# Optimization experiments

Measured on AMD Instinct MI355X. Metric: run time of the kernel, lower is better.

Reference implementation:

```python
import jax, jax.numpy as jnp
import numpy as np

SCALE = 30.0
MARGIN = 0.5
COS_M = float(np.cos(MARGIN))
SIN_M = float(np.sin(MARGIN))
TH = float(np.cos(np.pi - MARGIN))
MM = float(np.sin(np.pi - MARGIN) * MARGIN)
LN_EPS = 1e-7

B, S, H = 16, 2048, 1024
N_SPANS = 64
N_CLASSES = 4096


def setup_inputs() -> dict:
    key = jax.random.key(0)
    k1, k2, k3, k4, k5 = jax.random.split(key, 5)
    encoder_layer = jax.random.normal(k1, (B, S, H), dtype=jnp.float32)
    ln_gamma = jnp.ones((H,), jnp.float32)
    ln_beta = jnp.zeros((H,), jnp.float32)
    # xavier-uniform-like init for arcface head weight [out, in]
    limit = float(np.sqrt(6.0 / (N_CLASSES + H)))
    arc_weight = jax.random.uniform(k2, (N_CLASSES, H), jnp.float32, -limit, limit)
    heads = jax.random.randint(k3, (B, N_SPANS), 0, S - 32).astype(jnp.int32)
    lens = jax.random.randint(k4, (B, N_SPANS), 1, 33).astype(jnp.int32)
    tails = heads + lens  # guaranteed head < tail <= S
    labels = jax.random.randint(k5, (B, N_SPANS), 0, N_CLASSES).astype(jnp.int32)
    return {
        "encoder_layer": encoder_layer,
        "ln_gamma": ln_gamma,
        "ln_beta": ln_beta,
        "arc_weight": arc_weight,
        "span_head_idxs": heads,
        "span_tail_idxs": tails,
        "labels": labels,
    }


def _span_mean(encoder_layer, heads, tails):
    # fused ragged segment-mean via inclusive prefix sums over the seq dim
    # csum: [B, S+1, H], csum[b, t] = sum of encoder_layer[b, :t]
    csum = jnp.concatenate(
        [jnp.zeros_like(encoder_layer[:, :1]), jnp.cumsum(encoder_layer, axis=1)], axis=1
    )
    gather = lambda idx: jnp.take_along_axis(csum, idx[:, :, None].astype(jnp.int32), axis=1)
    sums = gather(tails) - gather(heads)  # [B, n_spans, H]
    counts = (tails - heads).astype(encoder_layer.dtype)[:, :, None]
    return sums / counts


def _layer_norm(x, gamma, beta):
    mu = jnp.mean(x, axis=-1, keepdims=True)
    var = jnp.mean(jnp.square(x - mu), axis=-1, keepdims=True)
    return (x - mu) * jax.lax.rsqrt(var + LN_EPS) * gamma + beta


def _l2norm(x):
    return x / jnp.maximum(jnp.linalg.norm(x, axis=-1, keepdims=True), 1e-12)


def reference(encoder_layer, ln_gamma, ln_beta, arc_weight, span_head_idxs, span_tail_idxs, labels):
    emb = _span_mean(encoder_layer, span_head_idxs, span_tail_idxs)  # [B, n_spans, H]
    emb = _layer_norm(emb, ln_gamma, ln_beta)
    emb = emb.reshape(-1, emb.shape[-1])  # [B*n_spans, H]
    lab = labels.reshape(-1)
    # ArcMarginProduct: cosine similarity
    cosine = (_l2norm(emb) @ _l2norm(arc_weight).T).astype(jnp.float32)  # [N, C]
    sine = jnp.sqrt(jnp.clip(1.0 - jnp.square(cosine), 0.0))
    phi = cosine * COS_M - sine * SIN_M
    phi = jnp.where(cosine > TH, phi, cosine - MM)
    onehot = jax.nn.one_hot(lab, cosine.shape[-1], dtype=cosine.dtype)
    logits = (onehot * phi + (1.0 - onehot) * cosine) * SCALE
    # mean cross entropy (all labels valid, ignore_index unused)
    logp = jax.nn.log_softmax(logits, axis=-1)
    nll = -jnp.take_along_axis(logp, lab[:, None].astype(jnp.int32), axis=1)[:, 0]
    return jnp.mean(nll)
```

## Files before the change

kernel.cpp:

```cpp
#include <hip/hip_runtime.h>
#include <math.h>

#define B_     16
#define S_     2048
#define H_     1024
#define NS_    64
#define NC_    4096
#define NROWS  1024

#define SCALE_ 30.0f
#define COS_M_ 0.8775825618903728f
#define SIN_M_ 0.479425538604203f
#define TH_    (-0.8775825618903728f)
#define MM_    0.2397127693021015f
#define LN_EPS_ 1e-7f


__device__ __forceinline__ unsigned short f2bf(float f) {
    union { float f; unsigned int u; } v; v.f = f;
    unsigned int r = v.u + 0x7fffu + ((v.u >> 16) & 1u);
    return (unsigned short)(r >> 16);
}

__device__ __forceinline__ float block_sum(float v) {
    __shared__ float sb[4];
    #pragma unroll
    for (int off = 32; off > 0; off >>= 1) v += __shfl_down(v, off, 64);
    if ((threadIdx.x & 63) == 0) sb[threadIdx.x >> 6] = v;
    __syncthreads();
    float r = sb[0] + sb[1] + sb[2] + sb[3];
    __syncthreads();
    return r;
}

__device__ __forceinline__ float block_max(float v) {
    __shared__ float sb[4];
    #pragma unroll
    for (int off = 32; off > 0; off >>= 1) v = fmaxf(v, __shfl_down(v, off, 64));
    if ((threadIdx.x & 63) == 0) sb[threadIdx.x >> 6] = v;
    __syncthreads();
    float r = fmaxf(fmaxf(sb[0], sb[1]), fmaxf(sb[2], sb[3]));
    __syncthreads();
    return r;
}

__device__ __forceinline__ void gload16(const void* g, void* l) {
    __builtin_amdgcn_global_load_lds(
        (const __attribute__((address_space(1))) unsigned int*)g,
        (__attribute__((address_space(3))) unsigned int*)l,
        16, 0, 0);
}

typedef short bf16x8 __attribute__((ext_vector_type(8)));
typedef float f32x4  __attribute__((ext_vector_type(4)));

__global__ __launch_bounds__(256) void fused_norm_kernel(
    const float* __restrict__ enc,
    const float* __restrict__ gamma,
    const float* __restrict__ beta,
    const int*   __restrict__ heads,
    const int*   __restrict__ tails,
    const float* __restrict__ W,
    unsigned short* __restrict__ embn,
    unsigned short* __restrict__ Wn,
    unsigned int*   __restrict__ cnt)
{
    const int tid = threadIdx.x;
    if (blockIdx.x == 0 && tid == 0) *cnt = 0u;

    if (blockIdx.x < NROWS) {
        const int span = blockIdx.x;
        const int b    = span >> 6;
        const int head = heads[span];
        const int tail = tails[span];
        const int cnt_ = tail - head;

        const float4* base = (const float4*)(enc + ((size_t)b * S_ + head) * H_) + tid;
        float4 a0 = {0.f,0.f,0.f,0.f}, a1 = a0, a2 = a0, a3 = a0;
        int s = 0;
        for (; s + 4 <= cnt_; s += 4) {
            float4 x0 = base[(size_t)(s + 0) * (H_ / 4)];
            float4 x1 = base[(size_t)(s + 1) * (H_ / 4)];
            float4 x2 = base[(size_t)(s + 2) * (H_ / 4)];
            float4 x3 = base[(size_t)(s + 3) * (H_ / 4)];
            a0.x += x0.x; a0.y += x0.y; a0.z += x0.z; a0.w += x0.w;
            a1.x += x1.x; a1.y += x1.y; a1.z += x1.z; a1.w += x1.w;
            a2.x += x2.x; a2.y += x2.y; a2.z += x2.z; a2.w += x2.w;
            a3.x += x3.x; a3.y += x3.y; a3.z += x3.z; a3.w += x3.w;
        }
        for (; s < cnt_; ++s) {
            float4 x = base[(size_t)s * (H_ / 4)];
            a0.x += x.x; a0.y += x.y; a0.z += x.z; a0.w += x.w;
        }
        const float inv = 1.0f / (float)cnt_;
        float v0 = (a0.x + a1.x + a2.x + a3.x) * inv;
        float v1 = (a0.y + a1.y + a2.y + a3.y) * inv;
        float v2 = (a0.z + a1.z + a2.z + a3.z) * inv;
        float v3 = (a0.w + a1.w + a2.w + a3.w) * inv;

        float mu = block_sum(v0 + v1 + v2 + v3) * (1.0f / H_);
        float d0 = v0 - mu, d1 = v1 - mu, d2 = v2 - mu, d3 = v3 - mu;
        float var = block_sum(d0*d0 + d1*d1 + d2*d2 + d3*d3) * (1.0f / H_);
        float rstd = rsqrtf(var + LN_EPS_);

        const int h = tid * 4;
        float y0 = d0 * rstd * gamma[h+0] + beta[h+0];
        float y1 = d1 * rstd * gamma[h+1] + beta[h+1];
        float y2 = d2 * rstd * gamma[h+2] + beta[h+2];
        float y3 = d3 * rstd * gamma[h+3] + beta[h+3];

        float ss = block_sum(y0*y0 + y1*y1 + y2*y2 + y3*y3);
        float invn = 1.0f / fmaxf(sqrtf(ss), 1e-12f);

        ushort4 o;
        o.x = f2bf(y0 * invn); o.y = f2bf(y1 * invn);
        o.z = f2bf(y2 * invn); o.w = f2bf(y3 * invn);
        *(ushort4*)(embn + (size_t)span * H_ + h) = o;
    } else {
        const int row = blockIdx.x - NROWS;
        float4 x = ((const float4*)(W + (size_t)row * H_))[tid];
        float ss = block_sum(x.x*x.x + x.y*x.y + x.z*x.z + x.w*x.w);
        float invn = 1.0f / fmaxf(sqrtf(ss), 1e-12f);
        ushort4 o;
        o.x = f2bf(x.x * invn); o.y = f2bf(x.y * invn);
        o.z = f2bf(x.z * invn); o.w = f2bf(x.w * invn);
        *(ushort4*)(Wn + (size_t)row * H_ + tid * 4) = o;
    }
}

__global__ __launch_bounds__(512, 1) void gemm_kernel(
    const unsigned short* __restrict__ A,
    const unsigned short* __restrict__ Bw,
    float* __restrict__ C)
{
    __shared__ short As[3][128 * 64];
    __shared__ short Bs[3][128 * 64];

    const int bid = blockIdx.y * 8 + blockIdx.x;
    const int swz = (bid & 7) * 32 + (bid >> 3);
    const int m0  = (swz & 7) * 128;
    const int n0  = (swz >> 3) * 128;

    const int tid  = threadIdx.x;
    const int lane = tid & 63;
    const int w    = tid >> 6;
    const int wRow = (w >> 2) * 64;
    const int wCol = (w & 3) * 32;
    const int lrow = lane & 15;
    const int q    = lane >> 4;
    const int xr   = lrow & 7;

    f32x4 acc[4][2];
    #pragma unroll
    for (int i = 0; i < 4; ++i)
        #pragma unroll
        for (int j = 0; j < 2; ++j)
            acc[i][j] = (f32x4){0.f, 0.f, 0.f, 0.f};

    auto stage = [&](int bsel, int k0) {
        #pragma unroll
        for (int h = 0; h < 2; ++h) {
            const int s   = tid + h * 512;
            const int row = s >> 3;
            const int s16 = (s & 7) ^ (row & 7);
            gload16(A  + (size_t)(m0 + row) * 1024 + k0 + s16 * 8, &As[bsel][s * 8]);
            gload16(Bw + (size_t)(n0 + row) * 1024 + k0 + s16 * 8, &Bs[bsel][s * 8]);
        }
    };

    auto compute = [&](int bsel) {
        #pragma unroll
        for (int kk = 0; kk < 2; ++kk) {
            const int c16 = ((kk << 2) | q) ^ xr;
            bf16x8 af[4], bfr[2];
            #pragma unroll
            for (int i = 0; i < 4; ++i)
                af[i] = *(const bf16x8*)(&As[bsel][(wRow + i * 16 + lrow) * 64 + c16 * 8]);
            #pragma unroll
            for (int j = 0; j < 2; ++j)
                bfr[j] = *(const bf16x8*)(&Bs[bsel][(wCol + j * 16 + lrow) * 64 + c16 * 8]);
            #pragma unroll
            for (int i = 0; i < 4; ++i)
                #pragma unroll
                for (int j = 0; j < 2; ++j)
                    acc[i][j] = __builtin_amdgcn_mfma_f32_16x16x32_bf16(af[i], bfr[j], acc[i][j], 0, 0, 0);
        }
    };

    stage(0, 0);
    stage(1, 64);
    asm volatile("s_waitcnt vmcnt(4)" ::: "memory");
    __builtin_amdgcn_s_barrier();

    int cur = 0, nxt = 1, fut = 2;
    for (int t = 0; t < 14; ++t) {
        stage(fut, (t + 2) * 64);
        compute(cur);
        asm volatile("s_waitcnt vmcnt(4)" ::: "memory");
        __builtin_amdgcn_s_barrier();
        const int tmp = cur; cur = nxt; nxt = fut; fut = tmp;
    }
    compute(cur);
    asm volatile("s_waitcnt vmcnt(0)" ::: "memory");
    __builtin_amdgcn_s_barrier();
    compute(nxt);

    #pragma unroll
    for (int i = 0; i < 4; ++i) {
        const int rbase = m0 + wRow + i * 16 + q * 4;
        #pragma unroll
        for (int j = 0; j < 2; ++j) {
            const int col = n0 + wCol + j * 16 + lrow;
            #pragma unroll
            for (int r2 = 0; r2 < 4; ++r2)
                C[(size_t)(rbase + r2) * NC_ + col] = acc[i][j][r2];
        }
    }
}

__global__ __launch_bounds__(256) void ce_kernel(
    const float* __restrict__ cosine,
    const int*   __restrict__ labels,
    float* __restrict__ nll,
    float* __restrict__ out,
    unsigned int* __restrict__ cnt)
{
    __shared__ float s_lab;
    __shared__ int   s_last;
    const int row = blockIdx.x;
    const int lab = labels[row];
    const int tid = threadIdx.x;
    const float4* c4 = (const float4*)(cosine + (size_t)row * NC_);

    float vals[16];
    float m = -1e30f;
    #pragma unroll
    for (int t = 0; t < 4; ++t) {
        float4 x = c4[tid + t * 256];
        const int cbase = (tid + t * 256) * 4;
        float xs[4] = {x.x, x.y, x.z, x.w};
        #pragma unroll
        for (int k = 0; k < 4; ++k) {
            float c = xs[k];
            float logit = c;
            if (cbase + k == lab) {
                float sine = sqrtf(fmaxf(1.0f - c * c, 0.0f));
                float phi  = c * COS_M_ - sine * SIN_M_;
                logit = (c > TH_) ? phi : (c - MM_);
            }
            logit *= SCALE_;
            vals[t * 4 + k] = logit;
            if (cbase + k == lab) s_lab = logit;
            m = fmaxf(m, logit);
        }
    }
    float gm = block_max(m);
    float e = 0.f;
    #pragma unroll
    for (int t = 0; t < 16; ++t) e += expf(vals[t] - gm);
    float se = block_sum(e);

    if (tid == 0) {
        nll[row] = logf(se) + gm - s_lab;
        __threadfence();
        s_last = (atomicAdd(cnt, 1u) == NROWS - 1);
    }
    __syncthreads();
    if (s_last) {
        __threadfence();
        float s = 0.f;
        #pragma unroll
        for (int t = 0; t < 4; ++t) s += nll[tid + t * 256];
        float tot = block_sum(s);
        if (tid == 0) out[0] = tot * (1.0f / NROWS);
    }
}

extern "C" void kernel_launch(void* const* d_in, const int* in_sizes, int n_in,
                              void* d_out, int out_size, void* d_ws, size_t ws_size,
                              hipStream_t stream) {
    const float* enc    = (const float*)d_in[0];
    const float* gamma  = (const float*)d_in[1];
    const float* beta   = (const float*)d_in[2];
    const float* W      = (const float*)d_in[3];
    const int*   heads  = (const int*)d_in[4];
    const int*   tails  = (const int*)d_in[5];
    const int*   labels = (const int*)d_in[6];
    float* out = (float*)d_out;

    char* ws = (char*)d_ws;
    unsigned short* embn   = (unsigned short*)(ws);
    unsigned short* Wn     = (unsigned short*)(ws + (2u  << 20));
    float*          cosine = (float*)        (ws + (10u << 20));
    float*          nllbuf = (float*)        (ws + (26u << 20));
    unsigned int*   cnt    = (unsigned int*) (ws + (26u << 20) + 8192);

    fused_norm_kernel<<<NROWS + NC_, 256, 0, stream>>>(enc, gamma, beta, heads, tails, W, embn, Wn, cnt);
    dim3 g3(8, 32);
    gemm_kernel <<<g3,  512, 0, stream>>>(embn, Wn, cosine);
    ce_kernel   <<<NROWS, 256, 0, stream>>>(cosine, labels, nllbuf, out, cnt);
}
```

Measured before the change: 234.8 us.

## Restructure GEMM to 4 waves with 64x64 warp tiles and double buffering

The GEMM now runs 256-thread blocks in which each wave computes a 64x64 tile, up from 64x32, so each fragment loaded from LDS feeds more MFMAs. Shared-memory staging drops from triple to double buffering and waits on all outstanding loads before each barrier, which allows two blocks per CU. The LayerNorm gamma and beta reads are also vectorised into float4 loads. Fewer waves per block and a full vmcnt(0) wait may expose more load latency. The 256-tile grid is small relative to the CU count.

```diff
diff --git a/kernel.cpp b/kernel.cpp
--- a/kernel.cpp
+++ b/kernel.cpp
@@ -103,11 +103,12 @@
         float var = block_sum(d0*d0 + d1*d1 + d2*d2 + d3*d3) * (1.0f / H_);
         float rstd = rsqrtf(var + LN_EPS_);
 
-        const int h = tid * 4;
-        float y0 = d0 * rstd * gamma[h+0] + beta[h+0];
-        float y1 = d1 * rstd * gamma[h+1] + beta[h+1];
-        float y2 = d2 * rstd * gamma[h+2] + beta[h+2];
-        float y3 = d3 * rstd * gamma[h+3] + beta[h+3];
+        const float4 g4 = ((const float4*)gamma)[tid];
+        const float4 b4 = ((const float4*)beta)[tid];
+        float y0 = d0 * rstd * g4.x + b4.x;
+        float y1 = d1 * rstd * g4.y + b4.y;
+        float y2 = d2 * rstd * g4.z + b4.z;
+        float y3 = d3 * rstd * g4.w + b4.w;
 
         float ss = block_sum(y0*y0 + y1*y1 + y2*y2 + y3*y3);
         float invn = 1.0f / fmaxf(sqrtf(ss), 1e-12f);
@@ -115,7 +116,7 @@
         ushort4 o;
         o.x = f2bf(y0 * invn); o.y = f2bf(y1 * invn);
         o.z = f2bf(y2 * invn); o.w = f2bf(y3 * invn);
-        *(ushort4*)(embn + (size_t)span * H_ + h) = o;
+        *(ushort4*)(embn + (size_t)span * H_ + tid * 4) = o;
     } else {
         const int row = blockIdx.x - NROWS;
         float4 x = ((const float4*)(W + (size_t)row * H_))[tid];
@@ -128,13 +129,13 @@
     }
 }
 
-__global__ __launch_bounds__(512, 1) void gemm_kernel(
+__global__ __launch_bounds__(256, 2) void gemm_kernel(
     const unsigned short* __restrict__ A,
     const unsigned short* __restrict__ Bw,
     float* __restrict__ C)
 {
-    __shared__ short As[3][128 * 64];
-    __shared__ short Bs[3][128 * 64];
+    __shared__ short As[2][128 * 64];
+    __shared__ short Bs[2][128 * 64];
 
     const int bid = blockIdx.y * 8 + blockIdx.x;
     const int swz = (bid & 7) * 32 + (bid >> 3);
@@ -144,23 +145,23 @@
     const int tid  = threadIdx.x;
     const int lane = tid & 63;
     const int w    = tid >> 6;
-    const int wRow = (w >> 2) * 64;
-    const int wCol = (w & 3) * 32;
+    const int wm   = (w & 1) * 64;
+    const int wn   = (w >> 1) * 64;
     const int lrow = lane & 15;
     const int q    = lane >> 4;
     const int xr   = lrow & 7;
 
-    f32x4 acc[4][2];
+    f32x4 acc[4][4];
     #pragma unroll
     for (int i = 0; i < 4; ++i)
         #pragma unroll
-        for (int j = 0; j < 2; ++j)
+        for (int j = 0; j < 4; ++j)
             acc[i][j] = (f32x4){0.f, 0.f, 0.f, 0.f};
 
     auto stage = [&](int bsel, int k0) {
         #pragma unroll
-        for (int h = 0; h < 2; ++h) {
-            const int s   = tid + h * 512;
+        for (int h = 0; h < 4; ++h) {
+            const int s   = tid + h * 256;
             const int row = s >> 3;
             const int s16 = (s & 7) ^ (row & 7);
             gload16(A  + (size_t)(m0 + row) * 1024 + k0 + s16 * 8, &As[bsel][s * 8]);
@@ -172,45 +173,41 @@
         #pragma unroll
         for (int kk = 0; kk < 2; ++kk) {
             const int c16 = ((kk << 2) | q) ^ xr;
-            bf16x8 af[4], bfr[2];
+            bf16x8 af[4], bfr[4];
             #pragma unroll
             for (int i = 0; i < 4; ++i)
-                af[i] = *(const bf16x8*)(&As[bsel][(wRow + i * 16 + lrow) * 64 + c16 * 8]);
-            #pragma unroll
-            for (int j = 0; j < 2; ++j)
-                bfr[j] = *(const bf16x8*)(&Bs[bsel][(wCol + j * 16 + lrow) * 64 + c16 * 8]);
+                af[i] = *(const bf16x8*)(&As[bsel][(wm + i * 16 + lrow) * 64 + c16 * 8]);
+            #pragma unroll
+            for (int j = 0; j < 4; ++j)
+                bfr[j] = *(const bf16x8*)(&Bs[bsel][(wn + j * 16 + lrow) * 64 + c16 * 8]);
             #pragma unroll
             for (int i = 0; i < 4; ++i)
                 #pragma unroll
-                for (int j = 0; j < 2; ++j)
+                for (int j = 0; j < 4; ++j)
                     acc[i][j] = __builtin_amdgcn_mfma_f32_16x16x32_bf16(af[i], bfr[j], acc[i][j], 0, 0, 0);
         }
     };
 
     stage(0, 0);
-    stage(1, 64);
-    asm volatile("s_waitcnt vmcnt(4)" ::: "memory");
-    __builtin_amdgcn_s_barrier();
-
-    int cur = 0, nxt = 1, fut = 2;
-    for (int t = 0; t < 14; ++t) {
-        stage(fut, (t + 2) * 64);
-        compute(cur);
-        asm volatile("s_waitcnt vmcnt(4)" ::: "memory");
-        __builtin_amdgcn_s_barrier();
-        const int tmp = cur; cur = nxt; nxt = fut; fut = tmp;
-    }
-    compute(cur);
     asm volatile("s_waitcnt vmcnt(0)" ::: "memory");
     __builtin_amdgcn_s_barrier();
-    compute(nxt);
+
+    int cur = 0;
+    for (int t = 0; t < 15; ++t) {
+        stage(cur ^ 1, (t + 1) * 64);
+        compute(cur);
+        asm volatile("s_waitcnt vmcnt(0)" ::: "memory");
+        __builtin_amdgcn_s_barrier();
+        cur ^= 1;
+    }
+    compute(cur);
 
     #pragma unroll
     for (int i = 0; i < 4; ++i) {
-        const int rbase = m0 + wRow + i * 16 + q * 4;
-        #pragma unroll
-        for (int j = 0; j < 2; ++j) {
-            const int col = n0 + wCol + j * 16 + lrow;
+        const int rbase = m0 + wm + i * 16 + q * 4;
+        #pragma unroll
+        for (int j = 0; j < 4; ++j) {
+            const int col = n0 + wn + j * 16 + lrow;
             #pragma unroll
             for (int r2 = 0; r2 < 4; ++r2)
                 C[(size_t)(rbase + r2) * NC_ + col] = acc[i][j][r2];
@@ -297,6 +294,6 @@
 
     fused_norm_kernel<<<NROWS + NC_, 256, 0, stream>>>(enc, gamma, beta, heads, tails, W, embn, Wn, cnt);
     dim3 g3(8, 32);
-    gemm_kernel <<<g3,  512, 0, stream>>>(embn, Wn, cosine);
+    gemm_kernel <<<g3,  256, 0, stream>>>(embn, Wn, cosine);
     ce_kernel   <<<NROWS, 256, 0, stream>>>(cosine, labels, nllbuf, out, cnt);
 }
```

After: 239.7 us. +2.1%, slower.
